# Kernel optimization log

Hardware: AMD Instinct MI355X
Metric: run time of the kernel (lower is better)

The kernel has to match this reference:

```python
import jax, jax.numpy as jnp
import numpy as np

B = 64        # num_groups
G = 32        # group_size
D = 2000      # output dim (counts per bin/gene)
M = 16        # m_samples
E = 16        # noise_dim
DIN = 256
LAM = 1.0
TRUST = 0.25
SMOOTH = 1e-8
IPF_ITERS = 60
EPS = 1e-12


def _arch(x, noise, W, b):
    # simple linear architecture: concat(x, noise) @ W + b
    return jnp.concatenate([x, noise], axis=-1) @ W + b


def _loss(x, target, W, b, noise_loss):
    # replicate each row m times (unsqueeze(1).expand(...).reshape == repeat)
    x_rep = jnp.repeat(x, M, axis=0)                      # [n*M, DIN]
    pred = _arch(x_rep, noise_loss, W, b)                 # [n*M, D] (no act_fn in loss path)
    pred = pred.reshape(B, G, M, D).sum(axis=1)           # [B, M, D]
    term_conf = jnp.linalg.norm(pred - target[:, None, :], axis=2).mean(axis=1)  # [B]
    sq = jnp.sum(pred * pred, axis=2)                     # [B, M]
    inn = jnp.einsum('bmd,bnd->bmn', pred, pred)          # [B, M, M]
    sqd = jnp.clip(sq[:, :, None] + sq[:, None, :] - 2.0 * inn, 1e-6)
    d = jnp.sqrt(sqd)
    mask = 1.0 - jnp.eye(M, dtype=d.dtype)
    mean_pd = jnp.sum(d * mask, axis=(1, 2)) / (M * (M - 1))
    return jnp.mean(term_conf - (LAM / 2.0) * mean_pd)


def _ipf(x_pred, C):
    # KL/I-projection with row anchoring (keep_rows=True, trust_clip=0.25)
    y = jnp.clip(x_pred, 0.0)
    C = jnp.clip(C.astype(y.dtype), 0.0)
    R = y.sum(axis=2)                                     # [B, G] anchor row totals
    col_zero = (y.sum(axis=1) <= 0) & (C > 0)
    y = y + SMOOTH * col_zero[:, None, :].astype(y.dtype)
    row_zero = (y.sum(axis=2) <= 0) & (R > 0)
    y = y + SMOOTH * row_zero[:, :, None].astype(y.dtype)

    def body(_, y):
        col = jnp.clip(y.sum(axis=1), EPS)
        y = y * jnp.clip(C / col, 1.0 - TRUST, 1.0 + TRUST)[:, None, :]
        row = jnp.clip(y.sum(axis=2), EPS)
        y = y * jnp.clip(R / row, 1.0 - TRUST, 1.0 + TRUST)[:, :, None]
        return y

    y = jax.lax.fori_loop(0, IPF_ITERS, body, y)
    col = jnp.clip(y.sum(axis=1), EPS)
    return y * (C / col)[:, None, :]


def _rank(v, descending):
    # rank along last axis via double argsort (0 = first picked)
    order = jnp.argsort(-v if descending else v, axis=-1)
    return jnp.argsort(order, axis=-1)


def _round_to_targets(x, target_bd):
    # exact integerization across G per (B, D); jit-safe full-G rank replaces dynamic-k topk+scatter
    x = jnp.clip(x, 0.0)
    xf = jnp.floor(x)
    y = xf.astype(jnp.int32)                              # [B, G, D]
    frac = x - xf
    need = target_bd - y.sum(axis=1)                      # [B, D]
    pos = jnp.clip(need, 0)
    q = pos // G
    y = y + q[:, None, :]
    r = pos - q * G
    rank = _rank(jnp.transpose(frac, (0, 2, 1)), descending=True)   # [B, D, G]
    add = (rank < r[:, :, None]).astype(jnp.int32)
    y = y + jnp.transpose(add, (0, 2, 1))
    # negative residuals: remove from smallest frac among y > 0
    need = target_bd - y.sum(axis=1)
    neg = jnp.clip(-need, 0)
    neg = jnp.minimum(neg, y.sum(axis=1))
    q = neg // G
    y_before = y
    y = jnp.clip(y - q[:, None, :], 0)
    removed = (y_before - y).sum(axis=1)
    r = neg - removed
    frac_m = jnp.where(y > 0, frac, jnp.inf)
    rank = _rank(jnp.transpose(frac_m, (0, 2, 1)), descending=False)
    rem = (rank < r[:, :, None]).astype(jnp.int32)
    y = jnp.clip(y - jnp.transpose(rem, (0, 2, 1)), 0)
    return y


def setup_inputs() -> dict:
    key = jax.random.key(0)
    ks = jax.random.split(key, 6)
    x = jax.random.normal(ks[0], (B * G, DIN), dtype=jnp.float32)
    target = jax.random.uniform(ks[1], (B, D), dtype=jnp.float32) * 100.0
    target_sum = jax.random.randint(ks[2], (B, D), 0, 200, dtype=jnp.int32)
    W = jax.random.normal(ks[3], (DIN + E, D), dtype=jnp.float32) * 0.02
    b = jnp.zeros((D,), dtype=jnp.float32)
    noise_loss = jax.random.normal(ks[4], (B * G * M, E), dtype=jnp.float32)
    noise_sample = jax.random.normal(ks[5], (B * G, E), dtype=jnp.float32)
    return {"x": x, "target": target, "target_sum": target_sum, "W": W, "b": b,
            "noise_loss": noise_loss, "noise_sample": noise_sample}


def reference(x, target, target_sum, W, b, noise_loss, noise_sample):
    loss = _loss(x, target, W, b, noise_loss)
    # conditional_sample pipeline (no-grad in original): softplus act (min_value==0)
    x_pred = jax.nn.softplus(_arch(x, noise_sample, W, b)).reshape(B, G, D)
    y_float = _ipf(x_pred, target_sum.astype(jnp.float32))
    y_int = _round_to_targets(y_float, target_sum.astype(jnp.int32))
    return loss, y_int.reshape(B * G, D)
```

## Files before the change

kernel.cpp:

```cpp
#include <hip/hip_runtime.h>
#include <math.h>

#define NB   64
#define NG   32
#define ND   2000
#define NM   16
#define NE   16
#define NDIN 256
#define NK   272

__device__ __forceinline__ float clampf(float v, float lo, float hi) {
    return fminf(fmaxf(v, lo), hi);
}

__device__ __forceinline__ float softplusf(float v) {
    return (v > 20.f) ? v : log1pf(expf(v));
}

__device__ __forceinline__ float readlane_f(float v, int lane) {
    return __int_as_float(__builtin_amdgcn_readlane(__float_as_int(v), lane));
}

__device__ __forceinline__ float wave_sum32(float v[NG], int lane) {
    {   const bool hi = (lane & 32) != 0;
        #pragma unroll
        for (int k = 0; k < 16; ++k) {
            float s = hi ? v[k] : v[k + 16];
            float r = __shfl_xor(s, 32);
            v[k] = (hi ? v[k + 16] : v[k]) + r;
        }
    }
    {   const bool hi = (lane & 16) != 0;
        #pragma unroll
        for (int k = 0; k < 8; ++k) {
            float s = hi ? v[k] : v[k + 8];
            float r = __shfl_xor(s, 16);
            v[k] = (hi ? v[k + 8] : v[k]) + r;
        }
    }
    {   const bool hi = (lane & 8) != 0;
        #pragma unroll
        for (int k = 0; k < 4; ++k) {
            float s = hi ? v[k] : v[k + 4];
            float r = __shfl_xor(s, 8);
            v[k] = (hi ? v[k + 4] : v[k]) + r;
        }
    }
    {   const bool hi = (lane & 4) != 0;
        #pragma unroll
        for (int k = 0; k < 2; ++k) {
            float s = hi ? v[k] : v[k + 2];
            float r = __shfl_xor(s, 4);
            v[k] = (hi ? v[k + 2] : v[k]) + r;
        }
    }
    {   const bool hi = (lane & 2) != 0;
        float s = hi ? v[0] : v[1];
        float r = __shfl_xor(s, 2);
        v[0] = (hi ? v[1] : v[0]) + r;
    }
    v[0] += __shfl_xor(v[0], 1);
    return v[0];
}


__device__ __forceinline__ void ipf_path(
        const float* __restrict__ xp, const int* __restrict__ tsum,
        float* __restrict__ out, float* smem, int b, int t) {
    const int lane = t & 63, w = t >> 6;
    const int d0 = t * 4;
    const bool valid = (d0 < ND);
    const int g_own = (lane >> 1) & 31;

    float* wred = smem;

    float y0r[4][NG];
    #pragma unroll
    for (int g = 0; g < NG; ++g) {
        float4 v = make_float4(0.f, 0.f, 0.f, 0.f);
        if (valid) v = *(const float4*)(xp + (size_t)(b * NG + g) * ND + d0);
        y0r[0][g] = fmaxf(v.x, 0.f);
        y0r[1][g] = fmaxf(v.y, 0.f);
        y0r[2][g] = fmaxf(v.z, 0.f);
        y0r[3][g] = fmaxf(v.w, 0.f);
    }
    float Cc[4] = {0.f, 0.f, 0.f, 0.f};
    if (valid) {
        const int4 ci = *(const int4*)(tsum + (size_t)b * ND + d0);
        Cc[0] = (float)ci.x; Cc[1] = (float)ci.y; Cc[2] = (float)ci.z; Cc[3] = (float)ci.w;
    }
    float Ac[4] = {1.f, 1.f, 1.f, 1.f};
    float Bown = 1.f;
    float Rown;

    {
        float v[NG];
        #pragma unroll
        for (int g = 0; g < NG; ++g)
            v[g] = y0r[0][g] + y0r[1][g] + y0r[2][g] + y0r[3][g];
        const float tot = wave_sum32(v, lane);
        if ((lane & 1) == 0) wred[w * NG + g_own] = tot;
        __syncthreads();
        float s = 0.f;
        #pragma unroll
        for (int w2 = 0; w2 < 8; ++w2) s += wred[w2 * NG + g_own];
        Rown = s;
    }

    for (int q = 1; q <= 60; ++q) {
        float s0 = 0.f, s1 = 0.f, s2 = 0.f, s3 = 0.f;
        #pragma unroll
        for (int g = 0; g < NG; ++g) {
            const float bg = readlane_f(Bown, 2 * g);
            s0 += y0r[0][g] * bg; s1 += y0r[1][g] * bg;
            s2 += y0r[2][g] * bg; s3 += y0r[3][g] * bg;
        }
        Ac[0] *= clampf(Cc[0] / fmaxf(Ac[0] * s0, 1e-12f), 0.75f, 1.25f);
        Ac[1] *= clampf(Cc[1] / fmaxf(Ac[1] * s1, 1e-12f), 0.75f, 1.25f);
        Ac[2] *= clampf(Cc[2] / fmaxf(Ac[2] * s2, 1e-12f), 0.75f, 1.25f);
        Ac[3] *= clampf(Cc[3] / fmaxf(Ac[3] * s3, 1e-12f), 0.75f, 1.25f);
        float v[NG];
        #pragma unroll
        for (int g = 0; g < NG; ++g)
            v[g] = y0r[0][g] * Ac[0] + y0r[1][g] * Ac[1]
                 + y0r[2][g] * Ac[2] + y0r[3][g] * Ac[3];
        const float tot = wave_sum32(v, lane);
        const int buf = (q & 1) * (8 * NG);
        if ((lane & 1) == 0) wred[buf + w * NG + g_own] = tot;
        __syncthreads();
        float s = 0.f;
        #pragma unroll
        for (int w2 = 0; w2 < 8; ++w2) s += wred[buf + w2 * NG + g_own];
        Bown *= clampf(Rown / fmaxf(Bown * s, 1e-12f), 0.75f, 1.25f);
    }

    if (!valid) return;

    unsigned pk[NG];
    #pragma unroll
    for (int g = 0; g < NG; ++g) pk[g] = 0u;

    #pragma unroll
    for (int j = 0; j < 4; ++j) {
        float fr[NG];
        int   yv[NG];
        float s = 0.f;
        #pragma unroll
        for (int g = 0; g < NG; ++g) {
            const float z = y0r[j][g] * Ac[j] * readlane_f(Bown, 2 * g);
            fr[g] = z;
            s += z;
        }
        const float F = Cc[j] / fmaxf(s, 1e-12f);
        int isum = 0;
        #pragma unroll
        for (int g = 0; g < NG; ++g) {
            const float y = fr[g] * F;
            const float fl = floorf(y);
            yv[g] = (int)fl;
            fr[g] = y - fl;
            isum += yv[g];
        }
        const int Ci = (int)Cc[j];
        const int need = Ci - isum;
        const int pos = max(need, 0);
        const int q = pos >> 5;
        const int r = pos & 31;
        #pragma unroll
        for (int g = 0; g < NG; ++g) yv[g] += q;
        #pragma unroll
        for (int g = 0; g < NG; ++g) {
            int rank = 0;
            #pragma unroll
            for (int h = 0; h < NG; ++h) {
                if (h == g) continue;
                rank += (h < g) ? (fr[h] >= fr[g] ? 1 : 0) : (fr[h] > fr[g] ? 1 : 0);
            }
            if (rank < r) yv[g] += 1;
        }
        int neg = max(-need, 0);
        neg = min(neg, isum);
        if (__builtin_expect(neg > 0, 0)) {
            const int q2 = neg >> 5;
            int removed = 0;
            #pragma unroll
            for (int g = 0; g < NG; ++g) {
                const int yb = yv[g];
                const int yn = max(yb - q2, 0);
                removed += yb - yn;
                yv[g] = yn;
            }
            const int r2 = neg - removed;
            if (r2 > 0) {
                const float INF = __builtin_inff();
                #pragma unroll
                for (int g = 0; g < NG; ++g) {
                    const float fg = (yv[g] > 0) ? fr[g] : INF;
                    int rank = 0;
                    #pragma unroll
                    for (int h = 0; h < NG; ++h) {
                        if (h == g) continue;
                        const float fh = (yv[h] > 0) ? fr[h] : INF;
                        rank += (h < g) ? (fh <= fg ? 1 : 0) : (fh < fg ? 1 : 0);
                    }
                    if (rank < r2) yv[g] = max(yv[g] - 1, 0);
                }
            }
        }
        #pragma unroll
        for (int g = 0; g < NG; ++g)
            pk[g] |= ((unsigned)yv[g]) << (8 * j);
    }
    #pragma unroll
    for (int g = 0; g < NG; ++g) {
        float* op = &out[1 + (size_t)(b * NG + g) * ND + d0];
        op[0] = (float)(pk[g] & 0xffu);
        op[1] = (float)((pk[g] >> 8) & 0xffu);
        op[2] = (float)((pk[g] >> 16) & 0xffu);
        op[3] = (float)((pk[g] >> 24) & 0xffu);
    }
}

__device__ __forceinline__ void loss_path(
        const float* __restrict__ x, const float* __restrict__ nl,
        const float* __restrict__ tgt, const float* __restrict__ W,
        const float* __restrict__ bias, float* __restrict__ res2,
        float* smem, int cx, int b, int t) {
    float* xsl = smem;
    float* nsl = smem + 256;
    float* tgl = smem + 512;
    float* pt  = smem + 764;

    if (t < 256) {
        const float* xb = x + (size_t)b * NG * NDIN;
        float s = 0.f;
        for (int g = 0; g < NG; ++g) s += xb[g * NDIN + t];
        xsl[t] = s;
        const float* nb = nl + (size_t)b * NG * (NM * NE);
        float s2 = 0.f;
        for (int g = 0; g < NG; ++g) s2 += nb[g * (NM * NE) + t];
        nsl[t] = s2;
    }

    int tm = 0, tn = 0;
    if (t >= 16 && t < 152) {
        int p = t - 16;
        for (int m = 0; m < NM; ++m) {
            int c = NM - m;
            if (p < c) { tm = m; tn = m + p; break; }
            p -= c;
        }
    }
    __syncthreads();

    const int d = cx * 250 + t;
    if (t < 250) {
        tgl[t] = tgt[b * ND + d];
        float xw = 0.f;
        #pragma unroll 8
        for (int k = 0; k < NDIN; ++k) xw += xsl[k] * W[(size_t)k * ND + d];
        float we[NE];
        #pragma unroll
        for (int e = 0; e < NE; ++e) we[e] = W[(size_t)(NDIN + e) * ND + d];
        const float base0 = xw + (float)NG * bias[d];
        #pragma unroll
        for (int m = 0; m < NM; ++m) {
            float pm = base0;
            #pragma unroll
            for (int e = 0; e < NE; ++e) pm += nsl[m * NE + e] * we[e];
            pt[m * 252 + t] = pm;
        }
    }
    if (t < 32) {
        pt[(t >> 1) * 252 + 250 + (t & 1)] = 0.f;
        if (t < 2) tgl[250 + t] = 0.f;
    }
    __syncthreads();

    float acc = 0.f;
    if (t < 16) {
        const float4* pa  = (const float4*)&pt[t * 252];
        const float4* tga = (const float4*)&tgl[0];
        for (int i = 0; i < 63; ++i) {
            float4 pv = pa[i], tv = tga[i];
            float e0 = pv.x - tv.x, e1 = pv.y - tv.y, e2 = pv.z - tv.z, e3 = pv.w - tv.w;
            acc += e0 * e0 + e1 * e1 + e2 * e2 + e3 * e3;
        }
    } else if (t < 152) {
        const float4* pa = (const float4*)&pt[tm * 252];
        const float4* pb = (const float4*)&pt[tn * 252];
        for (int i = 0; i < 63; ++i) {
            float4 u = pa[i], v = pb[i];
            acc += u.x * v.x + u.y * v.y + u.z * v.z + u.w * v.w;
        }
    }
    if (t < 152) res2[((size_t)b * 8 + cx) * 152 + t] = acc;
}

extern "C" __global__ __launch_bounds__(512, 1)
void mega(const float* __restrict__ x, const float* __restrict__ nl,
          const float* __restrict__ tgt, const float* __restrict__ W,
          const float* __restrict__ bias, const float* __restrict__ xp,
          const int* __restrict__ tsum, float* __restrict__ out,
          float* __restrict__ res2) {
    __shared__ float smem[4800];
    const int bid = blockIdx.x;
    const int t = threadIdx.x;
    if (bid < NB) {
        ipf_path(xp, tsum, out, smem, bid, t);
    } else {
        const int q = bid - NB;
        loss_path(x, nl, tgt, W, bias, res2, smem, q & 7, q >> 3, t);
    }
}

extern "C" __global__ __launch_bounds__(64)
void k2b_combine(const float* __restrict__ res2, float* __restrict__ out) {
    const int b = blockIdx.x, t = threadIdx.x;
    __shared__ float res[152];
    for (int tau = t; tau < 152; tau += 64) {
        float s = 0.f;
        #pragma unroll
        for (int c = 0; c < 8; ++c) s += res2[((size_t)b * 8 + c) * 152 + tau];
        res[tau] = s;
    }
    __syncthreads();
    if (t == 0) {
        float conf = 0.f;
        for (int m = 0; m < NM; ++m) conf += sqrtf(res[m]);
        conf *= (1.f / NM);
        float pd = 0.f;
        for (int m = 0; m < NM; ++m) {
            const int offm = 16 + m * NM - m * (m - 1) / 2;
            const float sqm = res[offm];
            for (int n = m + 1; n < NM; ++n) {
                const int offn = 16 + n * NM - n * (n - 1) / 2;
                const float sqn = res[offn];
                const float inn = res[offm + (n - m)];
                pd += sqrtf(fmaxf(sqm + sqn - 2.f * inn, 1e-6f));
            }
        }
        pd = 2.f * pd / (float)(NM * (NM - 1));
        atomicAdd(out, (conf - 0.5f * pd) * (1.f / NB));
    }
}

extern "C" __global__ __launch_bounds__(256)
void k3_xpred(const float* __restrict__ x, const float* __restrict__ nsamp,
              const float* __restrict__ W, const float* __restrict__ bias,
              float* __restrict__ xp) {
    const int dx = blockIdx.x;
    const int rb = blockIdx.y;
    const int t  = threadIdx.x;
    __shared__ float xr[8][NK];
    #pragma unroll
    for (int r = 0; r < 8; ++r) {
        const int row = rb * 8 + r;
        xr[r][t] = x[(size_t)row * NDIN + t];
        if (t < NE) xr[r][NDIN + t] = nsamp[row * NE + t];
    }
    __syncthreads();
    if (t >= 250) return;
    const int d = dx * 500 + 2 * t;
    float acc[8][2];
    #pragma unroll
    for (int r = 0; r < 8; ++r) { acc[r][0] = 0.f; acc[r][1] = 0.f; }

    float2 wc[4], wn[4];
    #pragma unroll
    for (int kk = 0; kk < 4; ++kk)
        wc[kk] = *(const float2*)&W[(size_t)kk * ND + d];

    for (int k = 0; k < NK; k += 4) {
        if (k + 4 < NK) {
            #pragma unroll
            for (int kk = 0; kk < 4; ++kk)
                wn[kk] = *(const float2*)&W[(size_t)(k + 4 + kk) * ND + d];
        }
        #pragma unroll
        for (int r = 0; r < 8; ++r) {
            const float4 xv = *(const float4*)&xr[r][k];
            acc[r][0] += xv.x * wc[0].x + xv.y * wc[1].x + xv.z * wc[2].x + xv.w * wc[3].x;
            acc[r][1] += xv.x * wc[0].y + xv.y * wc[1].y + xv.z * wc[2].y + xv.w * wc[3].y;
        }
        #pragma unroll
        for (int kk = 0; kk < 4; ++kk) wc[kk] = wn[kk];
    }
    const float2 bv = *(const float2*)&bias[d];
    #pragma unroll
    for (int r = 0; r < 8; ++r) {
        float2 o;
        o.x = softplusf(acc[r][0] + bv.x);
        o.y = softplusf(acc[r][1] + bv.y);
        *(float2*)&xp[(size_t)(rb * 8 + r) * ND + d] = o;
    }
}

extern "C" void kernel_launch(void* const* d_in, const int* in_sizes, int n_in,
                              void* d_out, int out_size, void* d_ws, size_t ws_size,
                              hipStream_t stream) {
    const float* x     = (const float*)d_in[0];
    const float* tgt   = (const float*)d_in[1];
    const int*   tsum  = (const int*)d_in[2];
    const float* W     = (const float*)d_in[3];
    const float* bias  = (const float*)d_in[4];
    const float* nl    = (const float*)d_in[5];
    const float* nsamp = (const float*)d_in[6];
    float* out = (float*)d_out;
    float* xp  = (float*)d_ws;

    (void)in_sizes; (void)n_in; (void)out_size; (void)ws_size;

    const size_t XPB = (size_t)2048 * 2000 * 4;
    float* res2 = (float*)((char*)d_ws + XPB);

    hipMemsetAsync(d_out, 0, sizeof(float), stream);

    hipLaunchKernelGGL(k3_xpred, dim3(4, 256), dim3(256), 0, stream,
                       x, nsamp, W, bias, xp);
    hipLaunchKernelGGL(mega, dim3(NB + 512), dim3(512), 0, stream,
                       x, nl, tgt, W, bias, xp, tsum, out, res2);
    hipLaunchKernelGGL(k2b_combine, dim3(NB), dim3(64), 0, stream, res2, out);
}
```

Baseline: 322.0 us.

## Fuse x_pred GEMM into IPF blocks and collapse loss combine into one block

The separate k3_xpred kernel and its 16MB workspace round-trip are removed. Each IPF block now computes its group's 32x2000 softplus projection directly into registers, using x and noise staged in shared memory. The loss combine becomes a single-block kernel with a wave reduction, which drops the memset and atomicAdd. The trade-off is that the 64 IPF blocks each do a serial 272-deep GEMM with heavy register pressure, which may lengthen the critical path of those blocks.

```diff
diff --git a/kernel.cpp b/kernel.cpp
--- a/kernel.cpp
+++ b/kernel.cpp
@@ -9,6 +9,8 @@
 #define NDIN 256
 #define NK   272
 
+#define XR_OFF 512
+
 __device__ __forceinline__ float clampf(float v, float lo, float hi) {
     return fminf(fmaxf(v, lo), hi);
 }
@@ -65,24 +67,55 @@
 
 
 __device__ __forceinline__ void ipf_path(
-        const float* __restrict__ xp, const int* __restrict__ tsum,
-        float* __restrict__ out, float* smem, int b, int t) {
+        const float* __restrict__ x, const float* __restrict__ nsamp,
+        const float* __restrict__ W, const float* __restrict__ bias,
+        const int* __restrict__ tsum, float* __restrict__ out,
+        float* smem, int b, int t) {
     const int lane = t & 63, w = t >> 6;
     const int d0 = t * 4;
     const bool valid = (d0 < ND);
     const int g_own = (lane >> 1) & 31;
 
     float* wred = smem;
+    float* xr   = smem + XR_OFF;
+
+    for (int idx = t; idx < NG * NK; idx += 512) {
+        const int g = idx / NK, c = idx - g * NK;
+        const int row = b * NG + g;
+        xr[idx] = (c < NDIN) ? x[(size_t)row * NDIN + c]
+                             : nsamp[(size_t)row * NE + (c - NDIN)];
+    }
+    __syncthreads();
 
     float y0r[4][NG];
     #pragma unroll
-    for (int g = 0; g < NG; ++g) {
-        float4 v = make_float4(0.f, 0.f, 0.f, 0.f);
-        if (valid) v = *(const float4*)(xp + (size_t)(b * NG + g) * ND + d0);
-        y0r[0][g] = fmaxf(v.x, 0.f);
-        y0r[1][g] = fmaxf(v.y, 0.f);
-        y0r[2][g] = fmaxf(v.z, 0.f);
-        y0r[3][g] = fmaxf(v.w, 0.f);
+    for (int j = 0; j < 4; ++j)
+        #pragma unroll
+        for (int g = 0; g < NG; ++g) y0r[j][g] = 0.f;
+
+    if (valid) {
+        for (int k = 0; k < NK; k += 4) {
+            float4 wk[4];
+            #pragma unroll
+            for (int kk = 0; kk < 4; ++kk)
+                wk[kk] = *(const float4*)&W[(size_t)(k + kk) * ND + d0];
+            #pragma unroll
+            for (int g = 0; g < NG; ++g) {
+                const float4 xv = *(const float4*)&xr[g * NK + k];
+                y0r[0][g] += xv.x * wk[0].x + xv.y * wk[1].x + xv.z * wk[2].x + xv.w * wk[3].x;
+                y0r[1][g] += xv.x * wk[0].y + xv.y * wk[1].y + xv.z * wk[2].y + xv.w * wk[3].y;
+                y0r[2][g] += xv.x * wk[0].z + xv.y * wk[1].z + xv.z * wk[2].z + xv.w * wk[3].z;
+                y0r[3][g] += xv.x * wk[0].w + xv.y * wk[1].w + xv.z * wk[2].w + xv.w * wk[3].w;
+            }
+        }
+        const float4 bv = *(const float4*)&bias[d0];
+        #pragma unroll
+        for (int g = 0; g < NG; ++g) {
+            y0r[0][g] = fmaxf(softplusf(y0r[0][g] + bv.x), 0.f);
+            y0r[1][g] = fmaxf(softplusf(y0r[1][g] + bv.y), 0.f);
+            y0r[2][g] = fmaxf(softplusf(y0r[2][g] + bv.z), 0.f);
+            y0r[3][g] = fmaxf(softplusf(y0r[3][g] + bv.w), 0.f);
+        }
     }
     float Cc[4] = {0.f, 0.f, 0.f, 0.f};
     if (valid) {
@@ -300,32 +333,35 @@
 extern "C" __global__ __launch_bounds__(512, 1)
 void mega(const float* __restrict__ x, const float* __restrict__ nl,
           const float* __restrict__ tgt, const float* __restrict__ W,
-          const float* __restrict__ bias, const float* __restrict__ xp,
+          const float* __restrict__ bias, const float* __restrict__ nsamp,
           const int* __restrict__ tsum, float* __restrict__ out,
           float* __restrict__ res2) {
-    __shared__ float smem[4800];
+    __shared__ float smem[XR_OFF + NG * NK];
     const int bid = blockIdx.x;
     const int t = threadIdx.x;
     if (bid < NB) {
-        ipf_path(xp, tsum, out, smem, bid, t);
+        ipf_path(x, nsamp, W, bias, tsum, out, smem, bid, t);
     } else {
         const int q = bid - NB;
         loss_path(x, nl, tgt, W, bias, res2, smem, q & 7, q >> 3, t);
     }
 }
 
-extern "C" __global__ __launch_bounds__(64)
-void k2b_combine(const float* __restrict__ res2, float* __restrict__ out) {
-    const int b = blockIdx.x, t = threadIdx.x;
-    __shared__ float res[152];
-    for (int tau = t; tau < 152; tau += 64) {
+extern "C" __global__ __launch_bounds__(512)
+void k2b_single(const float* __restrict__ res2, float* __restrict__ out) {
+    __shared__ float ls[NB * 152];
+    const int t = threadIdx.x;
+    for (int idx = t; idx < NB * 152; idx += 512) {
+        const int b = idx / 152, tau = idx - b * 152;
         float s = 0.f;
         #pragma unroll
         for (int c = 0; c < 8; ++c) s += res2[((size_t)b * 8 + c) * 152 + tau];
-        res[tau] = s;
+        ls[idx] = s;
     }
     __syncthreads();
-    if (t == 0) {
+    float v = 0.f;
+    if (t < NB) {
+        const float* res = &ls[t * 152];
         float conf = 0.f;
         for (int m = 0; m < NM; ++m) conf += sqrtf(res[m]);
         conf *= (1.f / NM);
@@ -341,58 +377,12 @@
             }
         }
         pd = 2.f * pd / (float)(NM * (NM - 1));
-        atomicAdd(out, (conf - 0.5f * pd) * (1.f / NB));
-    }
-}
-
-extern "C" __global__ __launch_bounds__(256)
-void k3_xpred(const float* __restrict__ x, const float* __restrict__ nsamp,
-              const float* __restrict__ W, const float* __restrict__ bias,
-              float* __restrict__ xp) {
-    const int dx = blockIdx.x;
-    const int rb = blockIdx.y;
-    const int t  = threadIdx.x;
-    __shared__ float xr[8][NK];
-    #pragma unroll
-    for (int r = 0; r < 8; ++r) {
-        const int row = rb * 8 + r;
-        xr[r][t] = x[(size_t)row * NDIN + t];
-        if (t < NE) xr[r][NDIN + t] = nsamp[row * NE + t];
-    }
-    __syncthreads();
-    if (t >= 250) return;
-    const int d = dx * 500 + 2 * t;
-    float acc[8][2];
-    #pragma unroll
-    for (int r = 0; r < 8; ++r) { acc[r][0] = 0.f; acc[r][1] = 0.f; }
-
-    float2 wc[4], wn[4];
-    #pragma unroll
-    for (int kk = 0; kk < 4; ++kk)
-        wc[kk] = *(const float2*)&W[(size_t)kk * ND + d];
-
-    for (int k = 0; k < NK; k += 4) {
-        if (k + 4 < NK) {
-            #pragma unroll
-            for (int kk = 0; kk < 4; ++kk)
-                wn[kk] = *(const float2*)&W[(size_t)(k + 4 + kk) * ND + d];
-        }
-        #pragma unroll
-        for (int r = 0; r < 8; ++r) {
-            const float4 xv = *(const float4*)&xr[r][k];
-            acc[r][0] += xv.x * wc[0].x + xv.y * wc[1].x + xv.z * wc[2].x + xv.w * wc[3].x;
-            acc[r][1] += xv.x * wc[0].y + xv.y * wc[1].y + xv.z * wc[2].y + xv.w * wc[3].y;
-        }
-        #pragma unroll
-        for (int kk = 0; kk < 4; ++kk) wc[kk] = wn[kk];
-    }
-    const float2 bv = *(const float2*)&bias[d];
-    #pragma unroll
-    for (int r = 0; r < 8; ++r) {
-        float2 o;
-        o.x = softplusf(acc[r][0] + bv.x);
-        o.y = softplusf(acc[r][1] + bv.y);
-        *(float2*)&xp[(size_t)(rb * 8 + r) * ND + d] = o;
+        v = (conf - 0.5f * pd) * (1.f / NB);
+    }
+    if (t < 64) {
+        #pragma unroll
+        for (int o = 32; o >= 1; o >>= 1) v += __shfl_xor(v, o);
+        if (t == 0) out[0] = v;
     }
 }
 
@@ -406,19 +396,12 @@
     const float* bias  = (const float*)d_in[4];
     const float* nl    = (const float*)d_in[5];
     const float* nsamp = (const float*)d_in[6];
-    float* out = (float*)d_out;
-    float* xp  = (float*)d_ws;
+    float* out  = (float*)d_out;
+    float* res2 = (float*)d_ws;
 
     (void)in_sizes; (void)n_in; (void)out_size; (void)ws_size;
 
-    const size_t XPB = (size_t)2048 * 2000 * 4;
-    float* res2 = (float*)((char*)d_ws + XPB);
-
-    hipMemsetAsync(d_out, 0, sizeof(float), stream);
-
-    hipLaunchKernelGGL(k3_xpred, dim3(4, 256), dim3(256), 0, stream,
-                       x, nsamp, W, bias, xp);
     hipLaunchKernelGGL(mega, dim3(NB + 512), dim3(512), 0, stream,
-                       x, nl, tgt, W, bias, xp, tsum, out, res2);
-    hipLaunchKernelGGL(k2b_combine, dim3(NB), dim3(64), 0, stream, res2, out);
-}
+                       x, nl, tgt, W, bias, nsamp, tsum, out, res2);
+    hipLaunchKernelGGL(k2b_single, dim3(1), dim3(512), 0, stream, res2, out);
+}
```

After: 470.0 us. 1.46x slower.
